# Optimization experiments

Measured on AMD Instinct MI355X. Metric: run time of the kernel, lower is better.

Reference implementation:

```python
import jax, jax.numpy as jnp
import numpy as np

LAMBDA_A = 1.0
NUM_ITER = 3
K = 64
BN_EPS = 1e-5


def setup_inputs() -> dict:
    key = jax.random.key(0)
    ks = jax.random.split(key, 8)
    B, C, H, W = 16, 512, 64, 64
    x = jax.random.normal(ks[0], (B, C, H, W), dtype=jnp.float32)
    # codebook mu: init normal(std~sqrt(2/k)) then L2-normalize along dim=1 (k axis), as in torch init
    mu = jax.random.normal(ks[1], (C, K), dtype=jnp.float32) * np.sqrt(2.0 / K)
    mu = mu / jnp.maximum(jnp.linalg.norm(mu, axis=1, keepdims=True), 1e-12)
    # 1x1 convs expressed as (out, in) matrices
    stem_w = jax.random.normal(ks[2], (C, C), dtype=jnp.float32) * np.sqrt(2.0 / C)
    stem_b = jnp.zeros((C,), dtype=jnp.float32)
    head_w = jax.random.normal(ks[3], (C, C), dtype=jnp.float32) * np.sqrt(2.0 / C)
    head_b = jnp.zeros((C,), dtype=jnp.float32)
    bn_gamma = jnp.ones((C,), dtype=jnp.float32)
    bn_beta = jnp.zeros((C,), dtype=jnp.float32)
    return {"x": x, "mu": mu, "stem_w": stem_w, "stem_b": stem_b,
            "head_w": head_w, "head_b": head_b,
            "bn_gamma": bn_gamma, "bn_beta": bn_beta}


def _conv1x1(x, w, b):
    # x: (B,C,H,W), w: (O,C)
    return jnp.einsum('bchw,oc->bohw', x, w) + b[None, :, None, None]


def reference(x, mu, stem_w, stem_b, head_w, head_b, bn_gamma, bn_beta):
    B, C, H, W = x.shape
    N = H * W
    y = _conv1x1(x, stem_w, stem_b)                 # (B,C,H,W)
    yf = y.reshape(B, C, N).transpose(0, 2, 1)      # (B,N,C)

    mu_b = jnp.broadcast_to(mu[None], (B, C, K))    # (B,C,K)
    z = None
    for _ in range(NUM_ITER):
        z = jax.nn.softmax(LAMBDA_A * jnp.einsum('bnc,bck->bnk', yf, mu_b), axis=2)
        zn = z / (1e-6 + z.sum(axis=1, keepdims=True))
        mu_b = jnp.einsum('bnc,bnk->bck', yf, zn)
        mu_b = mu_b / jnp.maximum(jnp.linalg.norm(mu_b, axis=1, keepdims=True), 1e-12)

    # EM loop runs under no_grad in torch
    mu_b = jax.lax.stop_gradient(mu_b)
    z = jax.lax.stop_gradient(z)

    y2 = jnp.einsum('bck,bnk->bcn', mu_b, z).reshape(B, C, H, W)

    # head: ReLU -> 1x1 conv -> BatchNorm2d (training-mode batch stats)
    h = _conv1x1(jnp.maximum(y2, 0.0), head_w, head_b)
    mean = h.mean(axis=(0, 2, 3), keepdims=True)
    var = h.var(axis=(0, 2, 3), keepdims=True)
    h = (h - mean) * jax.lax.rsqrt(var + BN_EPS)
    h = h * bn_gamma[None, :, None, None] + bn_beta[None, :, None, None]

    return jnp.maximum(h + x, 0.0)
```

## Files before the change

### kernel.cpp

```cpp
#include <hip/hip_runtime.h>


typedef _Float16 half_t;
typedef _Float16 half4 __attribute__((ext_vector_type(4)));
typedef _Float16 half8 __attribute__((ext_vector_type(8)));
typedef float f32x4 __attribute__((ext_vector_type(4)));

#define GLD_LDS(gp, lp) __builtin_amdgcn_global_load_lds( \
    (const __attribute__((address_space(1))) void*)(gp),  \
    (__attribute__((address_space(3))) void*)(lp), 16, 0, 0)

constexpr int CB = 16;
constexpr int CC = 512;
constexpr int CN = 4096;
constexpr int CKK = 64;
constexpr long MALL = (long)CB * CN;

__device__ inline int swz8(int bid, int n) {
  return (bid & 7) * (n >> 3) + (bid >> 3);
}

__global__ __launch_bounds__(256) void prep(
    const float* __restrict__ stem_w, const float* __restrict__ head_w,
    const float* __restrict__ mu,
    half_t* __restrict__ swh, half_t* __restrict__ hwh,
    half_t* __restrict__ muT, half_t* __restrict__ muck)
{
  int i = blockIdx.x * 256 + threadIdx.x;
  swh[i] = (half_t)stem_w[i];
  hwh[i] = (half_t)head_w[i];
  if (i < CC * CKK) {
    int c = i >> 6, k = i & 63;
    half_t v = (half_t)mu[i];
    for (int b = 0; b < CB; ++b) {
      muT[(long)b * CKK * CC + (long)k * CC + c] = v;
      muck[(long)b * CC * CKK + i] = v;
    }
  }
}

__global__ __launch_bounds__(256) void xpose(
    const float* __restrict__ in, half_t* __restrict__ outT)
{
  __shared__ half_t t[64][65];
  const int s0 = blockIdx.x * 64, r0 = blockIdx.y * 64;
  const long bz = blockIdx.z;
  const float* ib = in + bz * (long)CC * CN;
  half_t* ob = outT + bz * (long)CC * CN;
  const int tid = threadIdx.x, cl = tid & 63, rw = tid >> 6;
#pragma unroll
  for (int it = 0; it < 16; ++it) {
    int r = it * 4 + rw;
    t[cl][r] = (half_t)ib[(long)(r0 + r) * CN + s0 + cl];
  }
  __syncthreads();
#pragma unroll
  for (int it = 0; it < 16; ++it) {
    int s = it * 4 + rw;
    ob[(long)(s0 + s) * CC + r0 + cl] = t[s][cl];
  }
}

template <int BM, int BN, int MODE, int EPI, bool SWZ>
__global__ __launch_bounds__(256) void gemm_abt(
    const half_t* __restrict__ A, const half_t* __restrict__ Bm,
    half_t* __restrict__ Co, half_t* __restrict__ CoT,
    float* __restrict__ Cacc, const float* __restrict__ bias,
    int M, int Nn, int Kk, int ksplit, long sA, long sB, long sC)
{
  constexpr int FM = BM / 32, FN = BN / 32;
  constexpr int STG = (BM + BN) * 64;
  constexpr int EPS = (EPI != 0) ? BN * (BM + 4) : 0;
  constexpr int TOT = STG > EPS ? STG : EPS;
  __shared__ __align__(16) half_t smem[TOT];
  half_t* lA = smem;
  half_t* lB = smem + BM * 64;

  const int tid = threadIdx.x, wid = tid >> 6, lane = tid & 63;
  int bid = blockIdx.x;
  if constexpr (SWZ) bid = swz8(bid, gridDim.x);
  const int tilesN = Nn / BN;
  const int tm = bid / tilesN, tn = bid % tilesN;
  const long bz = blockIdx.z;
  const half_t* Ab = A + bz * sA + (long)tm * BM * Kk;
  const half_t* Bb = Bm + bz * sB + (long)tn * BN * Kk;
  const int ksteps = Kk >> 6;
  const int per = ksteps / ksplit;
  const int ks0 = blockIdx.y * per, ks1 = ks0 + per;
  const int wr = wid >> 1, wc = wid & 1;

  f32x4 acc[FM][FN];
#pragma unroll
  for (int i = 0; i < FM; ++i)
#pragma unroll
    for (int j = 0; j < FN; ++j) acc[i][j] = f32x4{0.f, 0.f, 0.f, 0.f};

  for (int ks = ks0; ks < ks1; ++ks) {
    __syncthreads();
    {
      const half_t* ga = Ab + (long)ks * 64;
#pragma unroll
      for (int c = wid; c < BM / 8; c += 4) {
        const half_t* g = ga + (long)(c * 8 + (lane >> 3)) * Kk + (lane & 7) * 8;
        GLD_LDS(g, &lA[c * 512]);
      }
      const half_t* gb = Bb + (long)ks * 64;
#pragma unroll
      for (int c = wid; c < BN / 8; c += 4) {
        const half_t* g = gb + (long)(c * 8 + (lane >> 3)) * Kk + (lane & 7) * 8;
        GLD_LDS(g, &lB[c * 512]);
      }
    }
    __syncthreads();
#pragma unroll
    for (int kk = 0; kk < 2; ++kk) {
      half8 af[FM], bfr[FN];
#pragma unroll
      for (int i = 0; i < FM; ++i)
        af[i] = *(const half8*)&lA[(wr * (BM / 2) + i * 16 + (lane & 15)) * 64 +
                                   kk * 32 + (lane >> 4) * 8];
#pragma unroll
      for (int j = 0; j < FN; ++j)
        bfr[j] = *(const half8*)&lB[(wc * (BN / 2) + j * 16 + (lane & 15)) * 64 +
                                    kk * 32 + (lane >> 4) * 8];
#pragma unroll
      for (int i = 0; i < FM; ++i)
#pragma unroll
        for (int j = 0; j < FN; ++j)
          acc[i][j] = __builtin_amdgcn_mfma_f32_16x16x32_f16(af[i], bfr[j],
                                                             acc[i][j], 0, 0, 0);
    }
  }

  if constexpr (EPI != 0) {
    static_assert(BM == 128 && BN == 128, "LDS epilogue assumes 128x128");
    constexpr int PIT = BM + 4;
    half_t* ep = smem;
    __syncthreads();
#pragma unroll
    for (int j = 0; j < FN; ++j) {
      const int nl = wc * 64 + j * 16 + (lane & 15);
      float bv = 0.f;
      if constexpr (MODE & 1) bv = bias[tn * BN + nl];
#pragma unroll
      for (int i = 0; i < FM; ++i) {
        const int ml = wr * 64 + i * 16 + ((lane >> 4) << 2);
        half4 h;
#pragma unroll
        for (int r = 0; r < 4; ++r) {
          float v = acc[i][j][r] + bv;
          if constexpr (MODE & 2) v = fmaxf(v, 0.f);
          h[r] = (half_t)v;
        }
        *(half4*)&ep[nl * PIT + ml] = h;
      }
    }
    __syncthreads();
    const long rowbase = (long)tm * BM;
    if constexpr (EPI & 1) {
#pragma unroll
      for (int s = 0; s < 8; ++s) {
        const int q = tid + 256 * s;
        const int m = q & 127, cc = q >> 7;
        half8 v;
#pragma unroll
        for (int e = 0; e < 8; ++e) v[e] = ep[(cc * 8 + e) * PIT + m];
        *(half8*)&Co[bz * sC + (rowbase + m) * Nn + tn * BN + cc * 8] = v;
      }
    }
    if constexpr (EPI & 2) {
#pragma unroll
      for (int s = 0; s < 8; ++s) {
        const int q = tid + 256 * s;
        const int cl = q & 127, mc = q >> 7;
        half8 v = *(const half8*)&ep[cl * PIT + mc * 8];
        const long row = rowbase + mc * 8;
        const long b = row >> 12, nsp = row & 4095;
        *(half8*)&CoT[(b * Nn + tn * BN + cl) * 4096 + nsp] = v;
      }
    }
  } else {
#pragma unroll
    for (int j = 0; j < FN; ++j) {
      const int n = tn * BN + wc * (BN / 2) + j * 16 + (lane & 15);
      float bv = 0.f;
      if constexpr (MODE & 1) bv = bias[n];
#pragma unroll
      for (int i = 0; i < FM; ++i) {
        const int mbase = tm * BM + wr * (BM / 2) + i * 16 + ((lane >> 4) << 2);
#pragma unroll
        for (int r = 0; r < 4; ++r) {
          const long idx = bz * sC + (long)(mbase + r) * Nn + n;
          if constexpr ((MODE & 4) != 0) {
            atomicAdd(&Cacc[idx], acc[i][j][r]);
          } else {
            float v = acc[i][j][r] + bv;
            if constexpr ((MODE & 2) != 0) v = fmaxf(v, 0.f);
            Co[idx] = (half_t)v;
          }
        }
      }
    }
  }
}

__global__ __launch_bounds__(256) void s_softmax(
    const half_t* __restrict__ Yf, const half_t* __restrict__ muT,
    half_t* __restrict__ zp, half_t* __restrict__ zT)
{
  __shared__ __align__(16) union {
    struct { half_t a[128 * 64]; half_t b[64 * 64]; } st;
    struct { float s[128 * 65]; half_t zh[128 * 68]; } p2;
  } sm;
  const int tid = threadIdx.x, wid = tid >> 6, lane = tid & 63;
  const int tm = blockIdx.x;
  const long bz = blockIdx.z;
  const half_t* Ab = Yf + bz * (long)CN * CC + (long)tm * 128 * CC;
  const half_t* Bb = muT + bz * (long)CKK * CC;
  const int wr = wid >> 1, wc = wid & 1;

  f32x4 acc[4][2];
#pragma unroll
  for (int i = 0; i < 4; ++i)
#pragma unroll
    for (int j = 0; j < 2; ++j) acc[i][j] = f32x4{0.f, 0.f, 0.f, 0.f};

  for (int ks = 0; ks < 8; ++ks) {
    __syncthreads();
    {
      const half_t* ga = Ab + (long)ks * 64;
#pragma unroll
      for (int c = wid; c < 16; c += 4) {
        const half_t* g = ga + (long)(c * 8 + (lane >> 3)) * CC + (lane & 7) * 8;
        GLD_LDS(g, &sm.st.a[c * 512]);
      }
      const half_t* gb = Bb + (long)ks * 64;
#pragma unroll
      for (int c = wid; c < 8; c += 4) {
        const half_t* g = gb + (long)(c * 8 + (lane >> 3)) * CC + (lane & 7) * 8;
        GLD_LDS(g, &sm.st.b[c * 512]);
      }
    }
    __syncthreads();
#pragma unroll
    for (int kk = 0; kk < 2; ++kk) {
      half8 af[4], bfr[2];
#pragma unroll
      for (int i = 0; i < 4; ++i)
        af[i] = *(const half8*)&sm.st.a[(wr * 64 + i * 16 + (lane & 15)) * 64 +
                                        kk * 32 + (lane >> 4) * 8];
#pragma unroll
      for (int j = 0; j < 2; ++j)
        bfr[j] = *(const half8*)&sm.st.b[(wc * 32 + j * 16 + (lane & 15)) * 64 +
                                         kk * 32 + (lane >> 4) * 8];
#pragma unroll
      for (int i = 0; i < 4; ++i)
#pragma unroll
        for (int j = 0; j < 2; ++j)
          acc[i][j] = __builtin_amdgcn_mfma_f32_16x16x32_f16(af[i], bfr[j],
                                                             acc[i][j], 0, 0, 0);
    }
  }
  __syncthreads();
#pragma unroll
  for (int j = 0; j < 2; ++j)
#pragma unroll
    for (int i = 0; i < 4; ++i)
#pragma unroll
      for (int r = 0; r < 4; ++r) {
        int nl = wc * 32 + j * 16 + (lane & 15);
        int ml = wr * 64 + i * 16 + ((lane >> 4) << 2) + r;
        sm.p2.s[ml * 65 + nl] = acc[i][j][r];
      }
  __syncthreads();
  if (tid < 128) {
    float row[64];
    float mx = -1e30f;
#pragma unroll
    for (int k = 0; k < 64; ++k) { row[k] = sm.p2.s[tid * 65 + k]; mx = fmaxf(mx, row[k]); }
    float sum = 0.f;
#pragma unroll
    for (int k = 0; k < 64; ++k) { row[k] = __expf(row[k] - mx); sum += row[k]; }
    const float inv = 1.f / sum;
#pragma unroll
    for (int k = 0; k < 64; ++k) sm.p2.zh[tid * 68 + k] = (half_t)(row[k] * inv);
  }
  __syncthreads();
  if (zp) {
    const int nl = tid >> 1, seg = tid & 1;
    const long base = bz * (long)CN * CKK + (long)(tm * 128 + nl) * CKK + seg * 32;
#pragma unroll
    for (int g = 0; g < 4; ++g) {
      half8 v;
#pragma unroll
      for (int e = 0; e < 8; ++e) v[e] = sm.p2.zh[nl * 68 + seg * 32 + g * 8 + e];
      *(half8*)&zp[base + g * 8] = v;
    }
  }
  {
    const int k = tid >> 2, seg = tid & 3;
    const long base = bz * (long)CKK * CN + (long)k * CN + tm * 128 + seg * 32;
#pragma unroll
    for (int g = 0; g < 4; ++g) {
      half8 v;
#pragma unroll
      for (int e = 0; e < 8; ++e) v[e] = sm.p2.zh[(seg * 32 + g * 8 + e) * 68 + k];
      *(half8*)&zT[base + g * 8] = v;
    }
  }
}

__global__ __launch_bounds__(64) void mu_norm(
    const float* __restrict__ acc, half_t* __restrict__ muT, half_t* __restrict__ muck)
{
  const int bk = blockIdx.x;
  const int b = bk >> 6, k = bk & 63;
  const float* row = acc + (long)bk * CC;
  const int t = threadIdx.x;
  float v[8]; float s = 0.f;
#pragma unroll
  for (int e = 0; e < 8; ++e) { v[e] = row[t * 8 + e]; s += v[e] * v[e]; }
#pragma unroll
  for (int m = 1; m < 64; m <<= 1) s += __shfl_xor(s, m);
  const float inv = 1.f / fmaxf(sqrtf(s), 1e-12f);
  half8 o;
#pragma unroll
  for (int e = 0; e < 8; ++e) o[e] = (half_t)(v[e] * inv);
  *(half8*)&muT[(long)bk * CC + t * 8] = o;
  half_t* mc = muck + (long)b * CC * CKK;
#pragma unroll
  for (int e = 0; e < 8; ++e) mc[(long)(t * 8 + e) * CKK + k] = o[e];
}

__global__ __launch_bounds__(256) void bn_stats2(
    const half_t* __restrict__ hcn, float* __restrict__ stats)
{
  const int c = blockIdx.x, tid = threadIdx.x;
  float s = 0.f, s2 = 0.f;
  for (int b = 0; b < CB; ++b) {
    const half_t* p = hcn + ((long)b * CC + c) * CN;
    for (int i = tid * 8; i < CN; i += 2048) {
      half8 v = *(const half8*)&p[i];
#pragma unroll
      for (int e = 0; e < 8; ++e) { float f = (float)v[e]; s += f; s2 += f * f; }
    }
  }
#pragma unroll
  for (int m = 1; m < 64; m <<= 1) { s += __shfl_xor(s, m); s2 += __shfl_xor(s2, m); }
  __shared__ float r[8];
  const int wid = tid >> 6;
  if ((tid & 63) == 0) { r[wid] = s; r[4 + wid] = s2; }
  __syncthreads();
  if (tid == 0) {
    stats[c] = r[0] + r[1] + r[2] + r[3];
    stats[CC + c] = r[4] + r[5] + r[6] + r[7];
  }
}

__global__ void bn_param(const float* __restrict__ stats,
                         const float* __restrict__ gamma, const float* __restrict__ beta,
                         float* __restrict__ scsh)
{
  const int c = threadIdx.x;
  const float cnt = 1.f / 65536.f;
  const float mean = stats[c] * cnt;
  const float var = stats[CC + c] * cnt - mean * mean;
  const float sc = gamma[c] * rsqrtf(var + 1e-5f);
  scsh[c] = sc;
  scsh[CC + c] = beta[c] - mean * sc;
}

__global__ __launch_bounds__(256) void bn_final2(
    const half_t* __restrict__ hcn, const float* __restrict__ x,
    const float* __restrict__ scsh, float* __restrict__ out)
{
  const long i8 = (long)blockIdx.x * 256 + threadIdx.x;
  const int c = (int)((i8 >> 9) & 511);
  const float sc = scsh[c], sh = scsh[CC + c];
  half8 h = *(const half8*)&hcn[i8 * 8];
  f32x4 x0 = *(const f32x4*)&x[i8 * 8];
  f32x4 x1 = *(const f32x4*)&x[i8 * 8 + 4];
  f32x4 o0, o1;
#pragma unroll
  for (int e = 0; e < 4; ++e) o0[e] = fmaxf((float)h[e] * sc + sh + x0[e], 0.f);
#pragma unroll
  for (int e = 0; e < 4; ++e) o1[e] = fmaxf((float)h[4 + e] * sc + sh + x1[e], 0.f);
  *(f32x4*)&out[i8 * 8] = o0;
  *(f32x4*)&out[i8 * 8 + 4] = o1;
}

extern "C" void kernel_launch(void* const* d_in, const int* in_sizes, int n_in,
                              void* d_out, int out_size, void* d_ws, size_t ws_size,
                              hipStream_t stream)
{
  const float* x      = (const float*)d_in[0];
  const float* mu     = (const float*)d_in[1];
  const float* stem_w = (const float*)d_in[2];
  const float* stem_b = (const float*)d_in[3];
  const float* head_w = (const float*)d_in[4];
  const float* head_b = (const float*)d_in[5];
  const float* bn_g   = (const float*)d_in[6];
  const float* bn_b   = (const float*)d_in[7];
  float* out = (float*)d_out;

  const size_t NEED = 214ull << 20;
  if (ws_size < NEED) {
    hipMemsetAsync(d_out, 0, (size_t)out_size * 4, stream);
    return;
  }
  char* ws = (char*)d_ws;
  const long MB = 1 << 20;
  half_t* xT   = (half_t*)(ws);
  half_t* Yf   = (half_t*)(ws + 64 * MB);
  half_t* ycn  = (half_t*)(ws + 128 * MB);
  half_t* z    = (half_t*)(ws + 192 * MB);
  half_t* zT   = (half_t*)(ws + 200 * MB);
  half_t* muT  = (half_t*)(ws + 208 * MB);
  half_t* muck = (half_t*)(ws + 209 * MB);
  float* muacc = (float*)(ws + 210 * MB);
  half_t* swh  = (half_t*)(ws + 212 * MB);
  half_t* hwh  = (half_t*)(ws + 212 * MB + 512 * 1024);
  float* stats = (float*)(ws + 213 * MB);
  float* scsh  = (float*)(ws + 213 * MB + 8 * 1024);
  half_t* y2f = xT;
  half_t* hcn = Yf;

  prep<<<1024, 256, 0, stream>>>(stem_w, head_w, mu, swh, hwh, muT, muck);
  xpose<<<dim3(64, 8, 16), 256, 0, stream>>>(x, xT);
  gemm_abt<128, 128, 1, 3, true><<<dim3(2048, 1, 1), 256, 0, stream>>>(
      xT, swh, Yf, ycn, nullptr, stem_b, (int)MALL, CC, CC, 1, 0, 0, 0);

  for (int it = 0; it < 3; ++it) {
    s_softmax<<<dim3(32, 1, 16), 256, 0, stream>>>(
        Yf, muT, (it == 2) ? z : nullptr, zT);
    hipMemsetAsync(muacc, 0, (size_t)CB * CKK * CC * 4, stream);
    gemm_abt<64, 128, 4, 0, false><<<dim3(4, 4, 16), 256, 0, stream>>>(
        zT, ycn, nullptr, nullptr, muacc, nullptr, CKK, CC, CN, 4,
        (long)CKK * CN, (long)CC * CN, (long)CKK * CC);
    mu_norm<<<CB * CKK, 64, 0, stream>>>(muacc, muT, muck);
  }
  gemm_abt<128, 128, 2, 1, true><<<dim3(128, 1, 16), 256, 0, stream>>>(
      z, muck, y2f, nullptr, nullptr, nullptr, CN, CC, CKK, 1,
      (long)CN * CKK, (long)CC * CKK, (long)CN * CC);
  gemm_abt<128, 128, 1, 2, true><<<dim3(2048, 1, 1), 256, 0, stream>>>(
      y2f, hwh, nullptr, hcn, nullptr, head_b, (int)MALL, CC, CC, 1, 0, 0, 0);

  bn_stats2<<<CC, 256, 0, stream>>>(hcn, stats);
  bn_param<<<1, 512, 0, stream>>>(stats, bn_g, bn_b, scsh);
  bn_final2<<<16384, 256, 0, stream>>>(hcn, x, scsh, out);
}
```

Baseline: 441.6 us.

## Double-buffer LDS staging in GEMMs and compute softmax in registers

The GEMM and scores kernels now use two LDS buffers, so the global-to-LDS load of the next K step is issued before the MFMAs of the current one, and only one barrier is needed per step. The softmax kernel changes its warp tiling so each wave owns full 64-column rows and does the row max and sum with cross-lane shuffles in registers. This removes the float scratch round trip through LDS and the step where only half the threads did a serial softmax. The transposed epilogue store is also re-indexed so consecutive threads write contiguous spans. In exchange, the doubled staging buffers use more LDS, which may lower occupancy.

```diff
diff --git a/kernel.cpp b/kernel.cpp
--- a/kernel.cpp
+++ b/kernel.cpp
@@ -69,12 +69,11 @@
     int M, int Nn, int Kk, int ksplit, long sA, long sB, long sC)
 {
   constexpr int FM = BM / 32, FN = BN / 32;
-  constexpr int STG = (BM + BN) * 64;
+  constexpr int HB = (BM + BN) * 64;
+  constexpr int STG = 2 * HB;
   constexpr int EPS = (EPI != 0) ? BN * (BM + 4) : 0;
   constexpr int TOT = STG > EPS ? STG : EPS;
   __shared__ __align__(16) half_t smem[TOT];
-  half_t* lA = smem;
-  half_t* lB = smem + BM * 64;
 
   const int tid = threadIdx.x, wid = tid >> 6, lane = tid & 63;
   int bid = blockIdx.x;
@@ -89,29 +88,32 @@
   const int ks0 = blockIdx.y * per, ks1 = ks0 + per;
   const int wr = wid >> 1, wc = wid & 1;
 
+  auto stage = [&](int ks, int buf) {
+    half_t* dA = smem + buf * HB;
+    half_t* dB = dA + BM * 64;
+    const half_t* ga = Ab + (long)ks * 64;
+#pragma unroll
+    for (int c = wid; c < BM / 8; c += 4)
+      GLD_LDS(ga + (long)(c * 8 + (lane >> 3)) * Kk + (lane & 7) * 8, &dA[c * 512]);
+    const half_t* gb = Bb + (long)ks * 64;
+#pragma unroll
+    for (int c = wid; c < BN / 8; c += 4)
+      GLD_LDS(gb + (long)(c * 8 + (lane >> 3)) * Kk + (lane & 7) * 8, &dB[c * 512]);
+  };
+
   f32x4 acc[FM][FN];
 #pragma unroll
   for (int i = 0; i < FM; ++i)
 #pragma unroll
     for (int j = 0; j < FN; ++j) acc[i][j] = f32x4{0.f, 0.f, 0.f, 0.f};
 
+  stage(ks0, 0);
+  __syncthreads();
+  int cur = 0;
   for (int ks = ks0; ks < ks1; ++ks) {
-    __syncthreads();
-    {
-      const half_t* ga = Ab + (long)ks * 64;
-#pragma unroll
-      for (int c = wid; c < BM / 8; c += 4) {
-        const half_t* g = ga + (long)(c * 8 + (lane >> 3)) * Kk + (lane & 7) * 8;
-        GLD_LDS(g, &lA[c * 512]);
-      }
-      const half_t* gb = Bb + (long)ks * 64;
-#pragma unroll
-      for (int c = wid; c < BN / 8; c += 4) {
-        const half_t* g = gb + (long)(c * 8 + (lane >> 3)) * Kk + (lane & 7) * 8;
-        GLD_LDS(g, &lB[c * 512]);
-      }
-    }
-    __syncthreads();
+    if (ks + 1 < ks1) stage(ks + 1, cur ^ 1);
+    const half_t* lA = smem + cur * HB;
+    const half_t* lB = lA + BM * 64;
 #pragma unroll
     for (int kk = 0; kk < 2; ++kk) {
       half8 af[FM], bfr[FN];
@@ -130,13 +132,14 @@
           acc[i][j] = __builtin_amdgcn_mfma_f32_16x16x32_f16(af[i], bfr[j],
                                                              acc[i][j], 0, 0, 0);
     }
+    __syncthreads();
+    cur ^= 1;
   }
 
   if constexpr (EPI != 0) {
     static_assert(BM == 128 && BN == 128, "LDS epilogue assumes 128x128");
     constexpr int PIT = BM + 4;
     half_t* ep = smem;
-    __syncthreads();
 #pragma unroll
     for (int j = 0; j < FN; ++j) {
       const int nl = wc * 64 + j * 16 + (lane & 15);
@@ -169,14 +172,14 @@
       }
     }
     if constexpr (EPI & 2) {
+      const long b = rowbase >> 12, nbase = rowbase & 4095;
 #pragma unroll
       for (int s = 0; s < 8; ++s) {
         const int q = tid + 256 * s;
-        const int cl = q & 127, mc = q >> 7;
+        const int mc = q & 15;
+        const int cl = q >> 4;
         half8 v = *(const half8*)&ep[cl * PIT + mc * 8];
-        const long row = rowbase + mc * 8;
-        const long b = row >> 12, nsp = row & 4095;
-        *(half8*)&CoT[(b * Nn + tn * BN + cl) * 4096 + nsp] = v;
+        *(half8*)&CoT[(b * Nn + tn * BN + cl) * 4096 + nbase + mc * 8] = v;
       }
     }
   } else {
@@ -208,83 +211,93 @@
     const half_t* __restrict__ Yf, const half_t* __restrict__ muT,
     half_t* __restrict__ zp, half_t* __restrict__ zT)
 {
+  constexpr int HB = (128 + 64) * 64;
   __shared__ __align__(16) union {
-    struct { half_t a[128 * 64]; half_t b[64 * 64]; } st;
-    struct { float s[128 * 65]; half_t zh[128 * 68]; } p2;
+    half_t st[2 * HB];
+    half_t zh[128 * 68];
   } sm;
   const int tid = threadIdx.x, wid = tid >> 6, lane = tid & 63;
   const int tm = blockIdx.x;
   const long bz = blockIdx.z;
   const half_t* Ab = Yf + bz * (long)CN * CC + (long)tm * 128 * CC;
   const half_t* Bb = muT + bz * (long)CKK * CC;
-  const int wr = wid >> 1, wc = wid & 1;
-
-  f32x4 acc[4][2];
-#pragma unroll
-  for (int i = 0; i < 4; ++i)
-#pragma unroll
-    for (int j = 0; j < 2; ++j) acc[i][j] = f32x4{0.f, 0.f, 0.f, 0.f};
-
+
+  auto stage = [&](int ks, int buf) {
+    half_t* dA = sm.st + buf * HB;
+    half_t* dB = dA + 128 * 64;
+    const half_t* ga = Ab + (long)ks * 64;
+#pragma unroll
+    for (int c = wid; c < 16; c += 4)
+      GLD_LDS(ga + (long)(c * 8 + (lane >> 3)) * CC + (lane & 7) * 8, &dA[c * 512]);
+    const half_t* gb = Bb + (long)ks * 64;
+#pragma unroll
+    for (int c = wid; c < 8; c += 4)
+      GLD_LDS(gb + (long)(c * 8 + (lane >> 3)) * CC + (lane & 7) * 8, &dB[c * 512]);
+  };
+
+  f32x4 acc[2][4];
+#pragma unroll
+  for (int i = 0; i < 2; ++i)
+#pragma unroll
+    for (int j = 0; j < 4; ++j) acc[i][j] = f32x4{0.f, 0.f, 0.f, 0.f};
+
+  stage(0, 0);
+  __syncthreads();
+  int cur = 0;
   for (int ks = 0; ks < 8; ++ks) {
-    __syncthreads();
-    {
-      const half_t* ga = Ab + (long)ks * 64;
-#pragma unroll
-      for (int c = wid; c < 16; c += 4) {
-        const half_t* g = ga + (long)(c * 8 + (lane >> 3)) * CC + (lane & 7) * 8;
-        GLD_LDS(g, &sm.st.a[c * 512]);
-      }
-      const half_t* gb = Bb + (long)ks * 64;
-#pragma unroll
-      for (int c = wid; c < 8; c += 4) {
-        const half_t* g = gb + (long)(c * 8 + (lane >> 3)) * CC + (lane & 7) * 8;
-        GLD_LDS(g, &sm.st.b[c * 512]);
-      }
-    }
-    __syncthreads();
+    if (ks + 1 < 8) stage(ks + 1, cur ^ 1);
+    const half_t* lA = sm.st + cur * HB;
+    const half_t* lB = lA + 128 * 64;
 #pragma unroll
     for (int kk = 0; kk < 2; ++kk) {
-      half8 af[4], bfr[2];
-#pragma unroll
-      for (int i = 0; i < 4; ++i)
-        af[i] = *(const half8*)&sm.st.a[(wr * 64 + i * 16 + (lane & 15)) * 64 +
-                                        kk * 32 + (lane >> 4) * 8];
-#pragma unroll
-      for (int j = 0; j < 2; ++j)
-        bfr[j] = *(const half8*)&sm.st.b[(wc * 32 + j * 16 + (lane & 15)) * 64 +
-                                         kk * 32 + (lane >> 4) * 8];
-#pragma unroll
-      for (int i = 0; i < 4; ++i)
-#pragma unroll
-        for (int j = 0; j < 2; ++j)
+      half8 af[2], bfr[4];
+#pragma unroll
+      for (int i = 0; i < 2; ++i)
+        af[i] = *(const half8*)&lA[(wid * 32 + i * 16 + (lane & 15)) * 64 +
+                                   kk * 32 + (lane >> 4) * 8];
+#pragma unroll
+      for (int j = 0; j < 4; ++j)
+        bfr[j] = *(const half8*)&lB[(j * 16 + (lane & 15)) * 64 +
+                                    kk * 32 + (lane >> 4) * 8];
+#pragma unroll
+      for (int i = 0; i < 2; ++i)
+#pragma unroll
+        for (int j = 0; j < 4; ++j)
           acc[i][j] = __builtin_amdgcn_mfma_f32_16x16x32_f16(af[i], bfr[j],
                                                              acc[i][j], 0, 0, 0);
     }
-  }
-  __syncthreads();
-#pragma unroll
-  for (int j = 0; j < 2; ++j)
-#pragma unroll
-    for (int i = 0; i < 4; ++i)
+    __syncthreads();
+    cur ^= 1;
+  }
+
+#pragma unroll
+  for (int i = 0; i < 2; ++i)
+#pragma unroll
+    for (int r = 0; r < 4; ++r) {
+      float mx = fmaxf(fmaxf(acc[i][0][r], acc[i][1][r]),
+                       fmaxf(acc[i][2][r], acc[i][3][r]));
+#pragma unroll
+      for (int m = 1; m < 16; m <<= 1) mx = fmaxf(mx, __shfl_xor(mx, m));
+      float p[4], s = 0.f;
+#pragma unroll
+      for (int j = 0; j < 4; ++j) { p[j] = __expf(acc[i][j][r] - mx); s += p[j]; }
+#pragma unroll
+      for (int m = 1; m < 16; m <<= 1) s += __shfl_xor(s, m);
+      const float inv = 1.f / s;
+#pragma unroll
+      for (int j = 0; j < 4; ++j) acc[i][j][r] = p[j] * inv;
+    }
+
+#pragma unroll
+  for (int i = 0; i < 2; ++i)
+#pragma unroll
+    for (int j = 0; j < 4; ++j)
 #pragma unroll
       for (int r = 0; r < 4; ++r) {
-        int nl = wc * 32 + j * 16 + (lane & 15);
-        int ml = wr * 64 + i * 16 + ((lane >> 4) << 2) + r;
-        sm.p2.s[ml * 65 + nl] = acc[i][j][r];
+        const int row = wid * 32 + i * 16 + ((lane >> 4) << 2) + r;
+        const int col = j * 16 + (lane & 15);
+        sm.zh[row * 68 + col] = (half_t)acc[i][j][r];
       }
-  __syncthreads();
-  if (tid < 128) {
-    float row[64];
-    float mx = -1e30f;
-#pragma unroll
-    for (int k = 0; k < 64; ++k) { row[k] = sm.p2.s[tid * 65 + k]; mx = fmaxf(mx, row[k]); }
-    float sum = 0.f;
-#pragma unroll
-    for (int k = 0; k < 64; ++k) { row[k] = __expf(row[k] - mx); sum += row[k]; }
-    const float inv = 1.f / sum;
-#pragma unroll
-    for (int k = 0; k < 64; ++k) sm.p2.zh[tid * 68 + k] = (half_t)(row[k] * inv);
-  }
   __syncthreads();
   if (zp) {
     const int nl = tid >> 1, seg = tid & 1;
@@ -293,7 +306,7 @@
     for (int g = 0; g < 4; ++g) {
       half8 v;
 #pragma unroll
-      for (int e = 0; e < 8; ++e) v[e] = sm.p2.zh[nl * 68 + seg * 32 + g * 8 + e];
+      for (int e = 0; e < 8; ++e) v[e] = sm.zh[nl * 68 + seg * 32 + g * 8 + e];
       *(half8*)&zp[base + g * 8] = v;
     }
   }
@@ -304,7 +317,7 @@
     for (int g = 0; g < 4; ++g) {
       half8 v;
 #pragma unroll
-      for (int e = 0; e < 8; ++e) v[e] = sm.p2.zh[(seg * 32 + g * 8 + e) * 68 + k];
+      for (int e = 0; e < 8; ++e) v[e] = sm.zh[(seg * 32 + g * 8 + e) * 68 + k];
       *(half8*)&zT[base + g * 8] = v;
     }
   }
```

Measured after the change: 431.0 us. -2.4%, faster.
